# Kernel optimization log

Hardware: AMD Instinct MI355X
Metric: run time of the kernel (lower is better)

## Reference

```python
import jax, jax.numpy as jnp
import numpy as np

EPS = 1e-12  # matches tf.nn.l2_normalize epsilon used by keras backend


def l2n(x, axis):
    return x / jnp.sqrt(jnp.maximum(jnp.sum(x * x, axis=axis, keepdims=True), EPS))


def setup_inputs() -> dict:
    key = jax.random.key(0)
    k1, k2, k3 = jax.random.split(key, 3)
    B, T, D, P = 32, 256, 512, 20
    inp_a = jax.random.normal(k1, (B, T, D), dtype=jnp.float32)
    inp_b = jax.random.normal(k2, (B, T, D), dtype=jnp.float32)
    # build(): output_dim weights of shape (1, D), 'uniform' init -> stacked (P, D)
    W = jax.random.uniform(k3, (P, D), dtype=jnp.float32, minval=-0.05, maxval=0.05)
    return {"inp_a": inp_a, "inp_b": inp_b, "W": W}


def reference(inp_a, inp_b, W):
    # l2-normalize over feature dim
    na = l2n(inp_a, -1)  # (B,T,D)
    nb = l2n(inp_b, -1)  # (B,T,D)
    # K.batch_dot(outp_b, outp_a, axes=[1,1]): contract seq axis -> (B,D,D)
    alpha = jnp.einsum('btd,bte->bde', nb, na)
    alpha = l2n(alpha, 1)
    # K.batch_dot(outp_b, alpha, axes=[2,1]): contract feature axis of b with axis1 of alpha -> (B,T,D)
    hmean = jnp.einsum('btd,bde->bte', nb, alpha)
    # per-perspective weighting + l2-normalize, vectorized over P perspectives
    aw = l2n(inp_a[:, :, None, :] * W[None, None, :, :], -1)   # (B,T,P,D)
    hw = l2n(hmean[:, :, None, :] * W[None, None, :, :], -1)   # (B,T,P,D)
    # batch_dot(hw_i, aw_i, axes=[2,2]) * eye summed == rowwise dot (diagonal only)
    persp = jnp.sum(aw * hw, axis=-1)  # (B,T,P)
    return (persp, persp)
```

## Files before the change

### kernel.cpp

```cpp
#include <hip/hip_runtime.h>

#define BB 32
#define TT 256
#define DD 512
#define PP 20
#define EPSF 1e-12f
#define BTP (BB * TT * PP)

typedef __attribute__((ext_vector_type(8))) short short8;
typedef __attribute__((ext_vector_type(4))) float f32x4;

__device__ inline unsigned short f2bf(float f) {
    unsigned u = __float_as_uint(f);
    u += 0x7fffu + ((u >> 16) & 1u);
    return (unsigned short)(u >> 16);
}
__device__ inline unsigned pack2(float lo, float hi) {
    return (unsigned)f2bf(lo) | ((unsigned)f2bf(hi) << 16);
}
__device__ inline float bf2f(unsigned s) {
    return __uint_as_float(s << 16);
}

union U8 { short8 s; uint4 u; };

__global__ __launch_bounds__(64)
void k_prep(const float* __restrict__ a, const float* __restrict__ b,
            float* __restrict__ inv_a,
            unsigned short* __restrict__ na_bf,
            unsigned short* __restrict__ nb_bf) {
    const int row  = blockIdx.x;
    const int lane = threadIdx.x;
    const float4* pa = (const float4*)(a + (size_t)row * DD);
    const float4* pb = (const float4*)(b + (size_t)row * DD);
    float4 a0 = pa[2 * lane], a1 = pa[2 * lane + 1];
    float4 b0 = pb[2 * lane], b1 = pb[2 * lane + 1];
    float sa = a0.x * a0.x + a0.y * a0.y + a0.z * a0.z + a0.w * a0.w
             + a1.x * a1.x + a1.y * a1.y + a1.z * a1.z + a1.w * a1.w;
    float sb = b0.x * b0.x + b0.y * b0.y + b0.z * b0.z + b0.w * b0.w
             + b1.x * b1.x + b1.y * b1.y + b1.z * b1.z + b1.w * b1.w;
#pragma unroll
    for (int off = 1; off < 64; off <<= 1) {
        sa += __shfl_xor(sa, off);
        sb += __shfl_xor(sb, off);
    }
    const float ia_ = rsqrtf(fmaxf(sa, EPSF));
    const float ib_ = rsqrtf(fmaxf(sb, EPSF));
    if (lane == 0) inv_a[row] = ia_;
    uint4 oa, ob;
    oa.x = pack2(a0.x * ia_, a0.y * ia_);
    oa.y = pack2(a0.z * ia_, a0.w * ia_);
    oa.z = pack2(a1.x * ia_, a1.y * ia_);
    oa.w = pack2(a1.z * ia_, a1.w * ia_);
    ob.x = pack2(b0.x * ib_, b0.y * ib_);
    ob.y = pack2(b0.z * ib_, b0.w * ib_);
    ob.z = pack2(b1.x * ib_, b1.y * ib_);
    ob.w = pack2(b1.z * ib_, b1.w * ib_);
    *(uint4*)(na_bf + (size_t)row * DD + 8 * lane) = oa;
    *(uint4*)(nb_bf + (size_t)row * DD + 8 * lane) = ob;
}

__global__ __launch_bounds__(256)
void k_mk_naT(const float* __restrict__ a, const float* __restrict__ inv_a,
              unsigned short* __restrict__ naT) {
    const int bz = blockIdx.z;
    const int e0 = blockIdx.x * 64;
    const int s0 = blockIdx.y * 64;
    __shared__ float Ts[64][65];
    const int tid = threadIdx.x;
    const float* ab = a + (size_t)bz * TT * DD;
#pragma unroll
    for (int i = 0; i < 4; ++i) {
        const int sr = (tid >> 4) + i * 16;
        const int ec = (tid & 15) * 4;
        float4 v = *(const float4*)(ab + (size_t)(s0 + sr) * DD + e0 + ec);
        const float s = inv_a[bz * TT + s0 + sr];
        Ts[sr][ec + 0] = v.x * s; Ts[sr][ec + 1] = v.y * s;
        Ts[sr][ec + 2] = v.z * s; Ts[sr][ec + 3] = v.w * s;
    }
    __syncthreads();
    unsigned short* nb = naT + (size_t)bz * DD * TT;
#pragma unroll
    for (int i = 0; i < 2; ++i) {
        const int el = (tid >> 3) + i * 32;
        const int s8 = (tid & 7) * 8;
        uint4 o;
        o.x = pack2(Ts[s8 + 0][el], Ts[s8 + 1][el]);
        o.y = pack2(Ts[s8 + 2][el], Ts[s8 + 3][el]);
        o.z = pack2(Ts[s8 + 4][el], Ts[s8 + 5][el]);
        o.w = pack2(Ts[s8 + 6][el], Ts[s8 + 7][el]);
        *(uint4*)(nb + (size_t)(e0 + el) * TT + s0 + s8) = o;
    }
}

__global__ __launch_bounds__(256)
void k_gemm_g(const unsigned short* __restrict__ nb,
              unsigned short* __restrict__ G) {
    const int bz = blockIdx.z;
    const int t0 = blockIdx.y * 64;
    const int s0 = blockIdx.x * 64;
    __shared__ __align__(16) unsigned short As[64 * 40];
    __shared__ __align__(16) unsigned short Bs[64 * 40];

    const int tid  = threadIdx.x;
    const int wave = tid >> 6, lane = tid & 63;
    const int quad = lane >> 4, ln = lane & 15;
    const int wm = wave >> 1, wn = wave & 1;

    const unsigned short* nbb = nb + (size_t)bz * TT * DD;

    const int lr = tid >> 2;
    const int c8 = (tid & 3) * 8;

    f32x4 acc[2][2];
#pragma unroll
    for (int i = 0; i < 2; ++i)
#pragma unroll
        for (int j = 0; j < 2; ++j)
#pragma unroll
            for (int r = 0; r < 4; ++r) acc[i][j][r] = 0.f;

    for (int k0 = 0; k0 < DD; k0 += 32) {
        *(uint4*)&As[lr * 40 + c8] =
            *(const uint4*)(nbb + (size_t)(t0 + lr) * DD + k0 + c8);
        *(uint4*)&Bs[lr * 40 + c8] =
            *(const uint4*)(nbb + (size_t)(s0 + lr) * DD + k0 + c8);
        __syncthreads();
        short8 af[2], bf[2];
        af[0] = *(const short8*)&As[(wm * 32 + ln) * 40 + quad * 8];
        af[1] = *(const short8*)&As[(wm * 32 + 16 + ln) * 40 + quad * 8];
        bf[0] = *(const short8*)&Bs[(wn * 32 + ln) * 40 + quad * 8];
        bf[1] = *(const short8*)&Bs[(wn * 32 + 16 + ln) * 40 + quad * 8];
#pragma unroll
        for (int i = 0; i < 2; ++i)
#pragma unroll
            for (int j = 0; j < 2; ++j)
                acc[i][j] = __builtin_amdgcn_mfma_f32_16x16x32_bf16(
                    af[i], bf[j], acc[i][j], 0, 0, 0);
        __syncthreads();
    }
    unsigned short* Gb = G + (size_t)bz * TT * TT;
#pragma unroll
    for (int i = 0; i < 2; ++i)
#pragma unroll
        for (int j = 0; j < 2; ++j) {
            const int col = s0 + wn * 32 + j * 16 + ln;
#pragma unroll
            for (int r = 0; r < 4; ++r) {
                const int row = t0 + wm * 32 + i * 16 + quad * 4 + r;
                Gb[(size_t)row * TT + col] = f2bf(acc[i][j][r]);
            }
        }
}

__global__ __launch_bounds__(256)
void k_gemm_h(const unsigned short* __restrict__ G,
              const unsigned short* __restrict__ naT,
              const unsigned short* __restrict__ na,
              unsigned short* __restrict__ H, float* __restrict__ q) {
    const int bz = blockIdx.z;
    const int t0 = blockIdx.y * 64;
    const int e0 = blockIdx.x * 64;
    __shared__ __align__(16) unsigned short As[64 * 40];
    __shared__ __align__(16) unsigned short Bs[64 * 40];
    __shared__ float qsum[64];

    const int tid  = threadIdx.x;
    const int wave = tid >> 6, lane = tid & 63;
    const int quad = lane >> 4, ln = lane & 15;
    const int wm = wave >> 1, wn = wave & 1;

    const unsigned short* Gb = G + (size_t)bz * TT * TT;
    const unsigned short* Nb = naT + (size_t)bz * DD * TT;

    const int lr = tid >> 2;
    const int c8 = (tid & 3) * 8;

    f32x4 acc[2][2];
#pragma unroll
    for (int i = 0; i < 2; ++i)
#pragma unroll
        for (int j = 0; j < 2; ++j)
#pragma unroll
            for (int r = 0; r < 4; ++r) acc[i][j][r] = 0.f;

    for (int k0 = 0; k0 < TT; k0 += 32) {
        *(uint4*)&As[lr * 40 + c8] =
            *(const uint4*)(Gb + (size_t)(t0 + lr) * TT + k0 + c8);
        *(uint4*)&Bs[lr * 40 + c8] =
            *(const uint4*)(Nb + (size_t)(e0 + lr) * TT + k0 + c8);
        __syncthreads();
        short8 af[2], bf[2];
        af[0] = *(const short8*)&As[(wm * 32 + ln) * 40 + quad * 8];
        af[1] = *(const short8*)&As[(wm * 32 + 16 + ln) * 40 + quad * 8];
        bf[0] = *(const short8*)&Bs[(wn * 32 + ln) * 40 + quad * 8];
        bf[1] = *(const short8*)&Bs[(wn * 32 + 16 + ln) * 40 + quad * 8];
#pragma unroll
        for (int i = 0; i < 2; ++i)
#pragma unroll
            for (int j = 0; j < 2; ++j)
                acc[i][j] = __builtin_amdgcn_mfma_f32_16x16x32_bf16(
                    af[i], bf[j], acc[i][j], 0, 0, 0);
        __syncthreads();
    }

    if (tid < 64) qsum[tid] = 0.f;
    __syncthreads();

    const unsigned short* nab = na + (size_t)bz * TT * DD;
    unsigned short* Hb = H + (size_t)bz * TT * DD;
#pragma unroll
    for (int j = 0; j < 2; ++j) {
        const int col = e0 + wn * 32 + j * 16 + ln;
        float qp = 0.f;
#pragma unroll
        for (int i = 0; i < 2; ++i) {
#pragma unroll
            for (int r = 0; r < 4; ++r) {
                const int row = t0 + wm * 32 + i * 16 + quad * 4 + r;
                const float hv = acc[i][j][r];
                Hb[(size_t)row * DD + col] = f2bf(hv);
                qp = fmaf(bf2f(nab[(size_t)row * DD + col]), hv, qp);
            }
        }
        qp += __shfl_xor(qp, 16);
        qp += __shfl_xor(qp, 32);
        if (quad == 0) atomicAdd(&qsum[wn * 32 + j * 16 + ln], qp);
    }
    __syncthreads();
    if (tid < 64) atomicAdd(q + bz * DD + e0 + tid, qsum[tid]);
}

__global__ __launch_bounds__(256)
void k_fin(const float* __restrict__ q, float* __restrict__ invq,
           const float* __restrict__ W, unsigned short* __restrict__ W2) {
    const int i = blockIdx.x * 256 + threadIdx.x;
    invq[i] = rsqrtf(fmaxf(q[i], EPSF));
    float w = (i < PP * DD) ? W[i] : 0.f;
    W2[i] = f2bf(w * w);
}

__global__ __launch_bounds__(64)
void k_persp_mfma(const unsigned short* __restrict__ na,
                  const unsigned short* __restrict__ H,
                  const float* __restrict__ invq,
                  const unsigned short* __restrict__ W2,
                  float* __restrict__ out) {
    const int b    = blockIdx.y;
    const int r0   = blockIdx.x * 16;
    const int lane = threadIdx.x;
    const int quad = lane >> 4, ln = lane & 15;
    const size_t rowbase = ((size_t)b * TT + r0 + ln) * DD;
    const float* iqb = invq + (size_t)b * DD;

    f32x4 s1[2], s2[2], s3[2];
#pragma unroll
    for (int j = 0; j < 2; ++j)
#pragma unroll
        for (int r = 0; r < 4; ++r) { s1[j][r] = 0.f; s2[j][r] = 0.f; s3[j][r] = 0.f; }

    for (int k0 = 0; k0 < DD; k0 += 32) {
        const int k = k0 + quad * 8;
        uint4 au = *(const uint4*)(na + rowbase + k);
        uint4 hu = *(const uint4*)(H + rowbase + k);
        float4 q0 = *(const float4*)(iqb + k);
        float4 q1 = *(const float4*)(iqb + k + 4);
        const float av[8] = {bf2f(au.x & 0xffffu), bf2f(au.x >> 16),
                             bf2f(au.y & 0xffffu), bf2f(au.y >> 16),
                             bf2f(au.z & 0xffffu), bf2f(au.z >> 16),
                             bf2f(au.w & 0xffffu), bf2f(au.w >> 16)};
        const float qv[8] = {q0.x, q0.y, q0.z, q0.w, q1.x, q1.y, q1.z, q1.w};
        float hv[8] = {bf2f(hu.x & 0xffffu), bf2f(hu.x >> 16),
                       bf2f(hu.y & 0xffffu), bf2f(hu.y >> 16),
                       bf2f(hu.z & 0xffffu), bf2f(hu.z >> 16),
                       bf2f(hu.w & 0xffffu), bf2f(hu.w >> 16)};
#pragma unroll
        for (int t = 0; t < 8; ++t) hv[t] *= qv[t];
        U8 ah, aa, hh;
        ah.u.x = pack2(av[0] * hv[0], av[1] * hv[1]);
        ah.u.y = pack2(av[2] * hv[2], av[3] * hv[3]);
        ah.u.z = pack2(av[4] * hv[4], av[5] * hv[5]);
        ah.u.w = pack2(av[6] * hv[6], av[7] * hv[7]);
        aa.u.x = pack2(av[0] * av[0], av[1] * av[1]);
        aa.u.y = pack2(av[2] * av[2], av[3] * av[3]);
        aa.u.z = pack2(av[4] * av[4], av[5] * av[5]);
        aa.u.w = pack2(av[6] * av[6], av[7] * av[7]);
        hh.u.x = pack2(hv[0] * hv[0], hv[1] * hv[1]);
        hh.u.y = pack2(hv[2] * hv[2], hv[3] * hv[3]);
        hh.u.z = pack2(hv[4] * hv[4], hv[5] * hv[5]);
        hh.u.w = pack2(hv[6] * hv[6], hv[7] * hv[7]);
        short8 bw0 = *(const short8*)(W2 + (size_t)ln * DD + k);
        short8 bw1 = *(const short8*)(W2 + (size_t)(16 + ln) * DD + k);
        s1[0] = __builtin_amdgcn_mfma_f32_16x16x32_bf16(ah.s, bw0, s1[0], 0, 0, 0);
        s1[1] = __builtin_amdgcn_mfma_f32_16x16x32_bf16(ah.s, bw1, s1[1], 0, 0, 0);
        s2[0] = __builtin_amdgcn_mfma_f32_16x16x32_bf16(aa.s, bw0, s2[0], 0, 0, 0);
        s2[1] = __builtin_amdgcn_mfma_f32_16x16x32_bf16(aa.s, bw1, s2[1], 0, 0, 0);
        s3[0] = __builtin_amdgcn_mfma_f32_16x16x32_bf16(hh.s, bw0, s3[0], 0, 0, 0);
        s3[1] = __builtin_amdgcn_mfma_f32_16x16x32_bf16(hh.s, bw1, s3[1], 0, 0, 0);
    }
#pragma unroll
    for (int j = 0; j < 2; ++j) {
        const int p = j * 16 + ln;
        if (p < PP) {
#pragma unroll
            for (int r = 0; r < 4; ++r) {
                const size_t row = (size_t)b * TT + r0 + quad * 4 + r;
                const float v = s1[j][r] * rsqrtf(fmaxf(s2[j][r], EPSF))
                                        * rsqrtf(fmaxf(s3[j][r], EPSF));
                out[row * PP + p] = v;
                out[(size_t)BTP + row * PP + p] = v;
            }
        }
    }
}

extern "C" void kernel_launch(void* const* d_in, const int* in_sizes, int n_in,
                              void* d_out, int out_size, void* d_ws, size_t ws_size,
                              hipStream_t stream) {
    (void)in_sizes; (void)n_in; (void)out_size; (void)ws_size;
    const float* a = (const float*)d_in[0];
    const float* b = (const float*)d_in[1];
    const float* W = (const float*)d_in[2];
    float* out = (float*)d_out;

    char* ws = (char*)d_ws;
    unsigned short* nb_bf = (unsigned short*)ws;
    unsigned short* naT   = (unsigned short*)(ws + (8u << 20));
    unsigned short* na_bf = (unsigned short*)(ws + (16u << 20));
    unsigned short* G_bf  = (unsigned short*)(ws + (24u << 20));
    unsigned short* H_bf  = (unsigned short*)(ws + (28u << 20));
    float* q     = (float*)(ws + (36u << 20));
    float* invq  = (float*)(ws + (36u << 20) + (64u << 10));
    unsigned short* W2 = (unsigned short*)(ws + (36u << 20) + (128u << 10));
    float* inv_a = (float*)(ws + (36u << 20) + (192u << 10));

    hipMemsetAsync(q, 0, (size_t)BB * DD * sizeof(float), stream);

    k_prep<<<BB * TT, 64, 0, stream>>>(a, b, inv_a, na_bf, nb_bf);

    dim3 gT(DD / 64, TT / 64, BB);
    k_mk_naT<<<gT, 256, 0, stream>>>(a, inv_a, naT);

    dim3 gG(TT / 64, TT / 64, BB);
    k_gemm_g<<<gG, 256, 0, stream>>>(nb_bf, G_bf);

    dim3 gH(DD / 64, TT / 64, BB);
    k_gemm_h<<<gH, 256, 0, stream>>>(G_bf, naT, na_bf, H_bf, q);

    k_fin<<<BB * DD / 256, 256, 0, stream>>>(q, invq, W, W2);

    dim3 gP(TT / 16, BB);
    k_persp_mfma<<<gP, 64, 0, stream>>>(na_bf, H_bf, invq, W2, out);
}
```

Baseline: 122.6 us.

## Fold memset and finalize kernel into neighbors; transpose from bf16 normalized A

Removes the hipMemsetAsync and the k_fin launch. The q zeroing and the W-squared conversion move into k_prep, and the rsqrt of q is computed per block into shared memory inside the perspective kernel. The transpose kernel now reads the already-normalized bf16 na (half the bytes of fp32 a) instead of re-reading fp32 a and inv_a. In exchange, every perspective block recomputes 512 rsqrts, and the transpose copies bf16 values directly rather than rounding the fp32 products itself.

```diff
diff --git a/kernel.cpp b/kernel.cpp
--- a/kernel.cpp
+++ b/kernel.cpp
@@ -26,9 +26,10 @@
 
 __global__ __launch_bounds__(64)
 void k_prep(const float* __restrict__ a, const float* __restrict__ b,
-            float* __restrict__ inv_a,
+            const float* __restrict__ W,
             unsigned short* __restrict__ na_bf,
-            unsigned short* __restrict__ nb_bf) {
+            unsigned short* __restrict__ nb_bf,
+            float* __restrict__ q, unsigned short* __restrict__ W2) {
     const int row  = blockIdx.x;
     const int lane = threadIdx.x;
     const float4* pa = (const float4*)(a + (size_t)row * DD);
@@ -46,7 +47,6 @@
     }
     const float ia_ = rsqrtf(fmaxf(sa, EPSF));
     const float ib_ = rsqrtf(fmaxf(sb, EPSF));
-    if (lane == 0) inv_a[row] = ia_;
     uint4 oa, ob;
     oa.x = pack2(a0.x * ia_, a0.y * ia_);
     oa.y = pack2(a0.z * ia_, a0.w * ia_);
@@ -58,38 +58,45 @@
     ob.w = pack2(b1.z * ib_, b1.w * ib_);
     *(uint4*)(na_bf + (size_t)row * DD + 8 * lane) = oa;
     *(uint4*)(nb_bf + (size_t)row * DD + 8 * lane) = ob;
+    if (lane < 2) {
+        const int i2 = 2 * row + lane;
+        q[i2] = 0.f;
+        const float w = (i2 < PP * DD) ? W[i2] : 0.f;
+        W2[i2] = f2bf(w * w);
+    }
 }
 
 __global__ __launch_bounds__(256)
-void k_mk_naT(const float* __restrict__ a, const float* __restrict__ inv_a,
-              unsigned short* __restrict__ naT) {
+void k_tr(const unsigned short* __restrict__ na,
+          unsigned short* __restrict__ naT) {
     const int bz = blockIdx.z;
     const int e0 = blockIdx.x * 64;
     const int s0 = blockIdx.y * 64;
-    __shared__ float Ts[64][65];
+    __shared__ unsigned int Ts[64][65];
     const int tid = threadIdx.x;
-    const float* ab = a + (size_t)bz * TT * DD;
-#pragma unroll
-    for (int i = 0; i < 4; ++i) {
-        const int sr = (tid >> 4) + i * 16;
-        const int ec = (tid & 15) * 4;
-        float4 v = *(const float4*)(ab + (size_t)(s0 + sr) * DD + e0 + ec);
-        const float s = inv_a[bz * TT + s0 + sr];
-        Ts[sr][ec + 0] = v.x * s; Ts[sr][ec + 1] = v.y * s;
-        Ts[sr][ec + 2] = v.z * s; Ts[sr][ec + 3] = v.w * s;
+    const unsigned short* nab = na + (size_t)bz * TT * DD;
+    unsigned short* naTb = naT + (size_t)bz * DD * TT;
+#pragma unroll
+    for (int i = 0; i < 2; ++i) {
+        const int s  = (tid >> 3) + i * 32;
+        const int e8 = (tid & 7) * 8;
+        uint4 v = *(const uint4*)(nab + (size_t)(s0 + s) * DD + e0 + e8);
+        Ts[s][e8 + 0] = v.x & 0xffffu; Ts[s][e8 + 1] = v.x >> 16;
+        Ts[s][e8 + 2] = v.y & 0xffffu; Ts[s][e8 + 3] = v.y >> 16;
+        Ts[s][e8 + 4] = v.z & 0xffffu; Ts[s][e8 + 5] = v.z >> 16;
+        Ts[s][e8 + 6] = v.w & 0xffffu; Ts[s][e8 + 7] = v.w >> 16;
     }
     __syncthreads();
-    unsigned short* nb = naT + (size_t)bz * DD * TT;
 #pragma unroll
     for (int i = 0; i < 2; ++i) {
         const int el = (tid >> 3) + i * 32;
         const int s8 = (tid & 7) * 8;
         uint4 o;
-        o.x = pack2(Ts[s8 + 0][el], Ts[s8 + 1][el]);
-        o.y = pack2(Ts[s8 + 2][el], Ts[s8 + 3][el]);
-        o.z = pack2(Ts[s8 + 4][el], Ts[s8 + 5][el]);
-        o.w = pack2(Ts[s8 + 6][el], Ts[s8 + 7][el]);
-        *(uint4*)(nb + (size_t)(e0 + el) * TT + s0 + s8) = o;
+        o.x = Ts[s8 + 0][el] | (Ts[s8 + 1][el] << 16);
+        o.y = Ts[s8 + 2][el] | (Ts[s8 + 3][el] << 16);
+        o.z = Ts[s8 + 4][el] | (Ts[s8 + 5][el] << 16);
+        o.w = Ts[s8 + 6][el] | (Ts[s8 + 7][el] << 16);
+        *(uint4*)(naTb + (size_t)(e0 + el) * TT + s0 + s8) = o;
     }
 }
 
@@ -231,19 +238,10 @@
     if (tid < 64) atomicAdd(q + bz * DD + e0 + tid, qsum[tid]);
 }
 
-__global__ __launch_bounds__(256)
-void k_fin(const float* __restrict__ q, float* __restrict__ invq,
-           const float* __restrict__ W, unsigned short* __restrict__ W2) {
-    const int i = blockIdx.x * 256 + threadIdx.x;
-    invq[i] = rsqrtf(fmaxf(q[i], EPSF));
-    float w = (i < PP * DD) ? W[i] : 0.f;
-    W2[i] = f2bf(w * w);
-}
-
 __global__ __launch_bounds__(64)
 void k_persp_mfma(const unsigned short* __restrict__ na,
                   const unsigned short* __restrict__ H,
-                  const float* __restrict__ invq,
+                  const float* __restrict__ q,
                   const unsigned short* __restrict__ W2,
                   float* __restrict__ out) {
     const int b    = blockIdx.y;
@@ -251,7 +249,22 @@
     const int lane = threadIdx.x;
     const int quad = lane >> 4, ln = lane & 15;
     const size_t rowbase = ((size_t)b * TT + r0 + ln) * DD;
-    const float* iqb = invq + (size_t)b * DD;
+
+    __shared__ float qs[DD];
+    {
+        const float* qb = q + (size_t)b * DD;
+        float4 v0 = *(const float4*)(qb + 8 * lane);
+        float4 v1 = *(const float4*)(qb + 8 * lane + 4);
+        qs[8 * lane + 0] = rsqrtf(fmaxf(v0.x, EPSF));
+        qs[8 * lane + 1] = rsqrtf(fmaxf(v0.y, EPSF));
+        qs[8 * lane + 2] = rsqrtf(fmaxf(v0.z, EPSF));
+        qs[8 * lane + 3] = rsqrtf(fmaxf(v0.w, EPSF));
+        qs[8 * lane + 4] = rsqrtf(fmaxf(v1.x, EPSF));
+        qs[8 * lane + 5] = rsqrtf(fmaxf(v1.y, EPSF));
+        qs[8 * lane + 6] = rsqrtf(fmaxf(v1.z, EPSF));
+        qs[8 * lane + 7] = rsqrtf(fmaxf(v1.w, EPSF));
+    }
+    __syncthreads();
 
     f32x4 s1[2], s2[2], s3[2];
 #pragma unroll
@@ -263,8 +276,8 @@
         const int k = k0 + quad * 8;
         uint4 au = *(const uint4*)(na + rowbase + k);
         uint4 hu = *(const uint4*)(H + rowbase + k);
-        float4 q0 = *(const float4*)(iqb + k);
-        float4 q1 = *(const float4*)(iqb + k + 4);
+        float4 q0 = *(const float4*)&qs[k];
+        float4 q1 = *(const float4*)&qs[k + 4];
         const float av[8] = {bf2f(au.x & 0xffffu), bf2f(au.x >> 16),
                              bf2f(au.y & 0xffffu), bf2f(au.y >> 16),
                              bf2f(au.z & 0xffffu), bf2f(au.z >> 16),
@@ -330,16 +343,12 @@
     unsigned short* G_bf  = (unsigned short*)(ws + (24u << 20));
     unsigned short* H_bf  = (unsigned short*)(ws + (28u << 20));
     float* q     = (float*)(ws + (36u << 20));
-    float* invq  = (float*)(ws + (36u << 20) + (64u << 10));
-    unsigned short* W2 = (unsigned short*)(ws + (36u << 20) + (128u << 10));
-    float* inv_a = (float*)(ws + (36u << 20) + (192u << 10));
-
-    hipMemsetAsync(q, 0, (size_t)BB * DD * sizeof(float), stream);
-
-    k_prep<<<BB * TT, 64, 0, stream>>>(a, b, inv_a, na_bf, nb_bf);
+    unsigned short* W2 = (unsigned short*)(ws + (36u << 20) + (64u << 10));
+
+    k_prep<<<BB * TT, 64, 0, stream>>>(a, b, W, na_bf, nb_bf, q, W2);
 
     dim3 gT(DD / 64, TT / 64, BB);
-    k_mk_naT<<<gT, 256, 0, stream>>>(a, inv_a, naT);
+    k_tr<<<gT, 256, 0, stream>>>(na_bf, naT);
 
     dim3 gG(TT / 64, TT / 64, BB);
     k_gemm_g<<<gG, 256, 0, stream>>>(nb_bf, G_bf);
@@ -347,8 +356,6 @@
     dim3 gH(DD / 64, TT / 64, BB);
     k_gemm_h<<<gH, 256, 0, stream>>>(G_bf, naT, na_bf, H_bf, q);
 
-    k_fin<<<BB * DD / 256, 256, 0, stream>>>(q, invq, W, W2);
-
     dim3 gP(TT / 16, BB);
-    k_persp_mfma<<<gP, 64, 0, stream>>>(na_bf, H_bf, invq, W2, out);
-}
+    k_persp_mfma<<<gP, 64, 0, stream>>>(na_bf, H_bf, q, W2, out);
+}
```

Result: faster. 118.2 us (-3.5%).
